# Kernel tuning notes

Measured on AMD Instinct MI355X. Metric: run time of the kernel, lower is better.

Reference implementation:

```python
import jax, jax.numpy as jnp
import numpy as np

N, E, H, F, ED, IN = 50000, 800000, 4, 32, 5, 256
NEG_SLOPE = 0.2


def setup_inputs() -> dict:
    key = jax.random.key(0)
    ks = jax.random.split(key, 13)
    s = 0.05
    return {
        "feat": jax.random.normal(ks[0], (N, IN), jnp.float32),
        "edge_fea": jax.random.normal(ks[1], (E, ED), jnp.float32),
        "src": jax.random.randint(ks[2], (E,), 0, N, dtype=jnp.int32),
        "dst": jax.random.randint(ks[3], (E,), 0, N, dtype=jnp.int32),
        "W_fc": jax.random.normal(ks[4], (IN, H * F), jnp.float32) * s,
        "W_edg": jax.random.normal(ks[5], (ED, H * ED), jnp.float32) * s,
        "b_edg": jnp.zeros((H * ED,), jnp.float32),
        "attn_l": jax.random.normal(ks[6], (1, H, F), jnp.float32) * s,
        "attn_r": jax.random.normal(ks[7], (1, H, F), jnp.float32) * s,
        "attn_edg": jax.random.normal(ks[8], (1, H, ED), jnp.float32) * s,
        "W_out": jax.random.normal(ks[9], (ED + F, F), jnp.float32) * s,
        "b_out": jnp.zeros((F,), jnp.float32),
        "bias": jnp.zeros((H * F,), jnp.float32),
    }


def reference(feat, edge_fea, src, dst, W_fc, W_edg, b_edg,
              attn_l, attn_r, attn_edg, W_out, b_out, bias):
    # node projection: [N, IN] -> [N, H, F]
    feat_src = (feat @ W_fc).reshape(N, H, F)
    # edge projection: [E, ED] -> [E, H, ED]
    efe = (edge_fea @ W_edg + b_edg).reshape(E, H, ED)
    # per-head attention logits
    el = (feat_src * attn_l).sum(-1)          # [N, H]
    er = (feat_src * attn_r).sum(-1)          # [N, H]
    ee = (efe * attn_edg).sum(-1)             # [E, H]
    e = jax.nn.leaky_relu(el[src] + er[dst] + ee, NEG_SLOPE)  # [E, H]
    # edge softmax over incoming edges of each dst node (numerically stable)
    m = jax.ops.segment_max(e, dst, num_segments=N)            # [N, H]
    ex = jnp.exp(e - m[dst])
    den = jax.ops.segment_sum(ex, dst, num_segments=N)         # [N, H]
    a = (ex / den[dst])[:, :, None]                            # [E, H, 1]
    # two weighted scatter-aggregations
    ft_f = jax.ops.segment_sum(a * efe, dst, num_segments=N)             # [N, H, ED]
    ft = jax.ops.segment_sum(a * feat_src[src], dst, num_segments=N)     # [N, H, F]
    rst = jnp.concatenate([ft_f, ft], axis=-1) @ W_out + b_out           # [N, H, F]
    rst = rst + bias.reshape(1, H, F)
    return rst
```

## Files before the change

kernel.cpp:

```cpp
#include <hip/hip_runtime.h>
#include <hip/hip_fp16.h>

#define N_NODES 50000
#define E_EDGES 800000
#define H_HEADS 4
#define F_FEAT 32
#define ED_DIM 5
#define IN_DIM 256
#define HF 128
#define NEG_SLOPE 0.2f
#define MAXD 64
#define PAYD 48
#define NPB 16
#define PROJ_BLOCKS 782
#define SCAT_BLOCKS 3125

typedef _Float16 half8 __attribute__((ext_vector_type(8)));
typedef float floatx4 __attribute__((ext_vector_type(4)));

__global__ __launch_bounds__(64) void k_wconv(
    const float* __restrict__ W_fc,
    _Float16* __restrict__ Whi, _Float16* __restrict__ Wlo,
    int* __restrict__ cnt)
{
    int b = blockIdx.x;
    int l = threadIdx.x;
    for (int i = b * 64 + l; i < N_NODES; i += 64 * 64) cnt[i] = 0;
    int kt = b >> 3, nt = b & 7;
    int kbase = kt * 32 + (l >> 4) * 8;
    int n = nt * 16 + (l & 15);
    half8 hi, lo;
#pragma unroll
    for (int j = 0; j < 8; ++j) {
        float w = W_fc[(kbase + j) * HF + n];
        _Float16 h = (_Float16)w;
        hi[j] = h;
        lo[j] = (_Float16)(w - (float)h);
    }
    size_t off = ((size_t)b * 64 + l) * 8;
    *(half8*)(Whi + off) = hi;
    *(half8*)(Wlo + off) = lo;
}

template <bool PAY>
__global__ __launch_bounds__(256) void k_scat(
    const int* __restrict__ dst,
    const int* __restrict__ src,
    const float* __restrict__ edge_fea,
    int* __restrict__ cnt,
    int* __restrict__ slots,
    char* __restrict__ pay)
{
    int e = blockIdx.x * 256 + threadIdx.x;
    if (e >= E_EDGES) return;
    int d = dst[e];
    if constexpr (PAY) {
        int s = src[e];
        const float* ep = edge_fea + (size_t)e * 5;
        float ef0 = ep[0], ef1 = ep[1], ef2 = ep[2], ef3 = ep[3], ef4 = ep[4];
        __half2 q01 = __floats2half2_rn(ef0, ef1);
        __half2 q23 = __floats2half2_rn(ef2, ef3);
        __half2 q4  = __floats2half2_rn(ef4, 0.f);
        int pos = atomicAdd(&cnt[d], 1);
        if (pos < PAYD) {
            uint4 v;
            v.x = *(unsigned*)&q01;
            v.y = *(unsigned*)&q23;
            v.z = *(unsigned*)&q4;
            v.w = (unsigned)s;
            *(uint4*)(pay + ((size_t)d * PAYD + pos) * 16) = v;
        }
    } else {
        int pos = atomicAdd(&cnt[d], 1);
        if (pos < MAXD) slots[(size_t)d * MAXD + pos] = e;
    }
}

__global__ __launch_bounds__(256) void k_proj(
    const float* __restrict__ feat,
    const _Float16* __restrict__ Whi,
    const _Float16* __restrict__ Wlo,
    const float* __restrict__ attn_l,
    const float* __restrict__ attn_r,
    __half2* __restrict__ feat_src,
    float* __restrict__ el,
    float* __restrict__ er)
{
    __shared__ _Float16 sC[4][16][136];

    int t = threadIdx.x;
    int lane = t & 63, wv = t >> 6;
    int l15 = lane & 15, lq = lane >> 4;
    int n0 = blockIdx.x * 64 + wv * 16;
    int arow = n0 + l15;
    int ar = arow < N_NODES ? arow : 0;

    floatx4 acc[8];
#pragma unroll
    for (int i = 0; i < 8; ++i) acc[i] = (floatx4){0.f, 0.f, 0.f, 0.f};

    const float4* Arow = (const float4*)(feat + (size_t)ar * IN_DIM);
    const half8* BH = (const half8*)Whi;
    const half8* BL = (const half8*)Wlo;
    int abase = lq * 2;

    for (int ks = 0; ks < 8; ++ks) {
        float4 a0 = Arow[ks * 8 + abase];
        float4 a1 = Arow[ks * 8 + abase + 1];
        float av[8] = {a0.x, a0.y, a0.z, a0.w, a1.x, a1.y, a1.z, a1.w};
        half8 ahi, alo;
#pragma unroll
        for (int j = 0; j < 8; ++j) {
            _Float16 h = (_Float16)av[j];
            ahi[j] = h;
            alo[j] = (_Float16)(av[j] - (float)h);
        }
#pragma unroll
        for (int tt = 0; tt < 8; ++tt) {
            half8 bh = BH[(ks * 8 + tt) * 64 + lane];
            half8 bl = BL[(ks * 8 + tt) * 64 + lane];
            acc[tt] = __builtin_amdgcn_mfma_f32_16x16x32_f16(ahi, bh, acc[tt], 0, 0, 0);
            acc[tt] = __builtin_amdgcn_mfma_f32_16x16x32_f16(alo, bh, acc[tt], 0, 0, 0);
            acc[tt] = __builtin_amdgcn_mfma_f32_16x16x32_f16(ahi, bl, acc[tt], 0, 0, 0);
        }
    }

#pragma unroll
    for (int tt = 0; tt < 8; ++tt) {
        int c = tt * 16 + l15;
#pragma unroll
        for (int r = 0; r < 4; ++r)
            sC[wv][lq * 4 + r][c] = (_Float16)acc[tt][r];
    }
    __syncthreads();

    int lr = lane >> 2;
    int hh = lane & 3;
    int n = n0 + lr;
    const _Float16* crow = &sC[wv][lr][hh * 32];
    const float* alp = attn_l + hh * 32;
    const float* arp = attn_r + hh * 32;
    float pl = 0.f, pr = 0.f;
#pragma unroll
    for (int i = 0; i < 32; ++i) {
        float v = (float)crow[i];
        pl += v * alp[i];
        pr += v * arp[i];
    }
    if (n < N_NODES) {
        el[n * H_HEADS + hh] = pl;
        er[n * H_HEADS + hh] = pr;
        uint4* po = (uint4*)(feat_src + (size_t)n * 64 + hh * 16);
        const uint4* ps = (const uint4*)crow;
        po[0] = ps[0]; po[1] = ps[1]; po[2] = ps[2]; po[3] = ps[3];
    }
}

__device__ __forceinline__ void acc8f(float* acc, uint4 v, float a) {
    float2 f;
    f = __half22float2(*(__half2*)&v.x); acc[0] += a * f.x; acc[1] += a * f.y;
    f = __half22float2(*(__half2*)&v.y); acc[2] += a * f.x; acc[3] += a * f.y;
    f = __half22float2(*(__half2*)&v.z); acc[4] += a * f.x; acc[5] += a * f.y;
    f = __half22float2(*(__half2*)&v.w); acc[6] += a * f.x; acc[7] += a * f.y;
}

template <bool PAY>
__global__ __launch_bounds__(256) void k_gather_out(
    const int* __restrict__ cnt, const int* __restrict__ slots,
    const char* __restrict__ pay,
    const int* __restrict__ src,
    const float* __restrict__ edge_fea,
    const float* __restrict__ el, const float* __restrict__ er,
    const __half2* __restrict__ feat_src,
    const float* __restrict__ W_edg, const float* __restrict__ b_edg,
    const float* __restrict__ attn_edg,
    const float* __restrict__ W_out, const float* __restrict__ b_out,
    const float* __restrict__ bias,
    float* __restrict__ out)
{
    constexpr int PD   = PAY ? PAYD : MAXD;
    constexpr int SAVR = PAY ? 200  : 264;
    constexpr int SSR  = PAY ? 50   : 66;

    __shared__ float sWe[100], sBe[20], sA[20], sWo[37 * 32], sBo[32], sBi[128];
    __shared__ __align__(16) __half          sav[NPB * SAVR];
    __shared__ __align__(16) unsigned short ssrc[NPB * SSR];
    __shared__ __align__(16) __half          sft[NPB * 136];
    int t = threadIdx.x;
    if (t < 100) sWe[t] = W_edg[t];
    if (t < 20) { sBe[t] = b_edg[t]; sA[t] = attn_edg[t]; }
    for (int i = t; i < 37 * 32; i += 256) sWo[i] = W_out[i];
    if (t < 32)  sBo[t] = b_out[t];
    if (t < 128) sBi[t] = bias[t];
    __syncthreads();

    int lane = t & 63;
    int wv   = t >> 6;
    int q    = lane >> 4;
    int ql   = lane & 15;
    int nb   = wv * 4 + q;
    int n    = blockIdx.x * NPB + nb;
    int h    = ql >> 2;

    int dq = cnt[n]; if (dq > PD) dq = PD;

    if (ql == 0) ssrc[nb * SSR] = 0;
    if (ql < 4)  sav[nb * SAVR + ql] = __float2half(0.f);

    float4 ern = ((const float4*)er)[n];

    float WA[5][4], cst[4];
#pragma unroll
    for (int hh = 0; hh < 4; hh++) {
        float c0 = 0.f;
#pragma unroll
        for (int dd = 0; dd < 5; dd++) c0 += sBe[hh * 5 + dd] * sA[hh * 5 + dd];
        cst[hh] = c0;
#pragma unroll
        for (int i = 0; i < 5; i++) {
            float w = 0.f;
#pragma unroll
            for (int dd = 0; dd < 5; dd++) w += sWe[i * 20 + hh * 5 + dd] * sA[hh * 5 + dd];
            WA[i][hh] = w;
        }
    }

    int dmax = dq;
    { int o = __shfl_xor(dmax, 16); dmax = dmax > o ? dmax : o;
      o = __shfl_xor(dmax, 32);     dmax = dmax > o ? dmax : o; }

    float sa4[4] = {0.f, 0.f, 0.f, 0.f};
    float m[20];
#pragma unroll
    for (int i = 0; i < 20; i++) m[i] = 0.f;

    for (int r = 0; r < dmax; r += 16) {
        int idx = r + ql;
        if (idx < dq) {
            float ef0, ef1, ef2, ef3, ef4;
            int s;
            if constexpr (PAY) {
                uint4 p = ((const uint4*)pay)[(size_t)n * PAYD + idx];
                float2 f01 = __half22float2(*(__half2*)&p.x);
                float2 f23 = __half22float2(*(__half2*)&p.y);
                float2 f4x = __half22float2(*(__half2*)&p.z);
                ef0 = f01.x; ef1 = f01.y; ef2 = f23.x; ef3 = f23.y; ef4 = f4x.x;
                s = (int)p.w;
            } else {
                int e = slots[(size_t)n * MAXD + idx];
                s = src[e];
                const float* ep = edge_fea + (size_t)e * 5;
                ef0 = ep[0]; ef1 = ep[1]; ef2 = ep[2]; ef3 = ep[3]; ef4 = ep[4];
            }
            float b0 = cst[0] + ef0*WA[0][0] + ef1*WA[1][0] + ef2*WA[2][0] + ef3*WA[3][0] + ef4*WA[4][0];
            float b1 = cst[1] + ef0*WA[0][1] + ef1*WA[1][1] + ef2*WA[2][1] + ef3*WA[3][1] + ef4*WA[4][1];
            float b2 = cst[2] + ef0*WA[0][2] + ef1*WA[1][2] + ef2*WA[2][2] + ef3*WA[3][2] + ef4*WA[4][2];
            float b3 = cst[3] + ef0*WA[0][3] + ef1*WA[1][3] + ef2*WA[2][3] + ef3*WA[3][3] + ef4*WA[4][3];
            float4 els = ((const float4*)el)[s];
            float lv0 = els.x + ern.x + b0;
            float lv1 = els.y + ern.y + b1;
            float lv2 = els.z + ern.z + b2;
            float lv3 = els.w + ern.w + b3;
            lv0 = lv0 >= 0.f ? lv0 : NEG_SLOPE * lv0;
            lv1 = lv1 >= 0.f ? lv1 : NEG_SLOPE * lv1;
            lv2 = lv2 >= 0.f ? lv2 : NEG_SLOPE * lv2;
            lv3 = lv3 >= 0.f ? lv3 : NEG_SLOPE * lv3;
            float a0 = __expf(lv0), a1 = __expf(lv1), a2 = __expf(lv2), a3 = __expf(lv3);
            sa4[0] += a0; sa4[1] += a1; sa4[2] += a2; sa4[3] += a3;
            m[0]  += a0 * ef0; m[1]  += a0 * ef1; m[2]  += a0 * ef2; m[3]  += a0 * ef3; m[4]  += a0 * ef4;
            m[5]  += a1 * ef0; m[6]  += a1 * ef1; m[7]  += a1 * ef2; m[8]  += a1 * ef3; m[9]  += a1 * ef4;
            m[10] += a2 * ef0; m[11] += a2 * ef1; m[12] += a2 * ef2; m[13] += a2 * ef3; m[14] += a2 * ef4;
            m[15] += a3 * ef0; m[16] += a3 * ef1; m[17] += a3 * ef2; m[18] += a3 * ef3; m[19] += a3 * ef4;
            ssrc[nb * SSR + idx] = (unsigned short)s;
            __half2 p01 = __floats2half2_rn(a0, a1);
            __half2 p23 = __floats2half2_rn(a2, a3);
            uint2 pk = make_uint2(*(unsigned*)&p01, *(unsigned*)&p23);
            *(uint2*)&sav[nb * SAVR + idx * 4] = pk;
        }
    }

    float acc[8];
#pragma unroll
    for (int k = 0; k < 8; k++) acc[k] = 0.f;
    const uint4* fs4 = (const uint4*)feat_src;
    int savb = nb * SAVR + h;
    int sib  = nb * SSR;

    for (int j = 0; j < dmax; j += 8) {
        int cc[8]; float aa[8]; int ss[8]; uint4 vv[8];
#pragma unroll
        for (int u = 0; u < 8; ++u) {
            int jj = j + u;
            cc[u] = (jj < dq) ? jj : 0;
            aa[u] = (jj < dq) ? __half2float(sav[savb + cc[u] * 4]) : 0.f;
        }
#pragma unroll
        for (int u = 0; u < 8; ++u) ss[u] = ssrc[sib + cc[u]];
#pragma unroll
        for (int u = 0; u < 8; ++u) vv[u] = fs4[(size_t)ss[u] * 16 + ql];
#pragma unroll
        for (int u = 0; u < 8; ++u) acc8f(acc, vv[u], aa[u]);
    }

#pragma unroll
    for (int off = 1; off < 16; off <<= 1) {
#pragma unroll
        for (int hh = 0; hh < 4; hh++) sa4[hh] += __shfl_xor(sa4[hh], off);
#pragma unroll
        for (int qq = 0; qq < 20; qq++) m[qq] += __shfl_xor(m[qq], off);
    }
    float rh = sa4[h] > 0.f ? 1.f / sa4[h] : 0.f;
#pragma unroll
    for (int k = 0; k < 8; k++) acc[k] *= rh;

    {
        __half2 h01 = __floats2half2_rn(acc[0], acc[1]);
        __half2 h23 = __floats2half2_rn(acc[2], acc[3]);
        __half2 h45 = __floats2half2_rn(acc[4], acc[5]);
        __half2 h67 = __floats2half2_rn(acc[6], acc[7]);
        uint4 pk = make_uint4(*(unsigned*)&h01, *(unsigned*)&h23,
                              *(unsigned*)&h45, *(unsigned*)&h67);
        *(uint4*)&sft[nb * 136 + 8 * ql] = pk;
    }

    float ftf[5];
#pragma unroll
    for (int d = 0; d < 5; d++) {
        float s = 0.f;
#pragma unroll
        for (int i = 0; i < 5; i++) s += m[h * 5 + i] * sWe[i * 20 + h * 5 + d];
        ftf[d] = (dq > 0) ? (sBe[h * 5 + d] + s * rh) : 0.f;
    }

    int f0 = 8 * (ql & 3);
    float o[8];
#pragma unroll
    for (int k = 0; k < 8; k++) {
        int f = f0 + k, cc = h * 32 + f;
        o[k] = sBo[f] + sBi[cc];
#pragma unroll
        for (int d = 0; d < 5; d++) o[k] += ftf[d] * sWo[d * 32 + f];
    }
    for (int g = 0; g < 32; g++) {
        float ftg = __half2float(sft[nb * 136 + h * 32 + g]);
#pragma unroll
        for (int k = 0; k < 8; k++) o[k] += ftg * sWo[(5 + g) * 32 + f0 + k];
    }
    float4* po = (float4*)(out + (size_t)n * HF + 8 * ql);
    po[0] = make_float4(o[0], o[1], o[2], o[3]);
    po[1] = make_float4(o[4], o[5], o[6], o[7]);
}

extern "C" void kernel_launch(void* const* d_in, const int* in_sizes, int n_in,
                              void* d_out, int out_size, void* d_ws, size_t ws_size,
                              hipStream_t stream) {
    const float* feat     = (const float*)d_in[0];
    const float* edge_fea = (const float*)d_in[1];
    const int*   src      = (const int*)d_in[2];
    const int*   dst      = (const int*)d_in[3];
    const float* W_fc     = (const float*)d_in[4];
    const float* W_edg    = (const float*)d_in[5];
    const float* b_edg    = (const float*)d_in[6];
    const float* attn_l   = (const float*)d_in[7];
    const float* attn_r   = (const float*)d_in[8];
    const float* attn_edg = (const float*)d_in[9];
    const float* W_out    = (const float*)d_in[10];
    const float* b_out    = (const float*)d_in[11];
    const float* bias     = (const float*)d_in[12];

    char* ws = (char*)d_ws;
    size_t off = 0;
    __half2* feat_src = (__half2*)(ws + off); off += (size_t)N_NODES * 128 * 2;
    float*   el       = (float*)(ws + off);   off += (size_t)N_NODES * 4 * 4;
    float*   er       = (float*)(ws + off);   off += (size_t)N_NODES * 4 * 4;
    int*     cnt      = (int*)(ws + off);     off += (size_t)N_NODES * 4;
    _Float16* Whi     = (_Float16*)(ws + off); off += 8 * 8 * 64 * 8 * 2;
    _Float16* Wlo     = (_Float16*)(ws + off); off += 8 * 8 * 64 * 8 * 2;
    size_t off_common = off;
    char* pay = ws + off_common;
    size_t need_pay = off_common + (size_t)N_NODES * PAYD * 16;
    int* slots = (int*)(ws + off_common);

    bool use_pay = ws_size >= need_pay;

    k_wconv<<<64, 64, 0, stream>>>(W_fc, Whi, Wlo, cnt);
    if (use_pay) {
        k_scat<true><<<SCAT_BLOCKS, 256, 0, stream>>>(dst, src, edge_fea, cnt, slots, pay);
        k_proj<<<PROJ_BLOCKS, 256, 0, stream>>>(feat, Whi, Wlo, attn_l, attn_r,
                                                feat_src, el, er);
        k_gather_out<true><<<N_NODES / NPB, 256, 0, stream>>>(
            cnt, slots, pay, src, edge_fea, el, er, feat_src,
            W_edg, b_edg, attn_edg, W_out, b_out, bias, (float*)d_out);
    } else {
        k_scat<false><<<SCAT_BLOCKS, 256, 0, stream>>>(dst, src, edge_fea, cnt, slots, pay);
        k_proj<<<PROJ_BLOCKS, 256, 0, stream>>>(feat, Whi, Wlo, attn_l, attn_r,
                                                feat_src, el, er);
        k_gather_out<false><<<N_NODES / NPB, 256, 0, stream>>>(
            cnt, slots, pay, src, edge_fea, el, er, feat_src,
            W_edg, b_edg, attn_edg, W_out, b_out, bias, (float*)d_out);
    }
}
```

Measured before the change: 283.3 us.

## Merge edge scatter and node projection into one launch with disjoint block ranges

The edge-bucketing scatter kernel and the node projection GEMM kernel become one kernel: the first block range does the scatter and the rest run the projection. The two independent stages can now overlap on the GPU and one launch gap goes away. Each scatter thread now handles four edges instead of one, with all loads issued before the atomics for more memory-level parallelism. The fused kernel carries the projection's shared-memory allocation for every block, which may lower occupancy for the scatter blocks.

```diff
diff --git a/kernel.cpp b/kernel.cpp
--- a/kernel.cpp
+++ b/kernel.cpp
@@ -13,7 +13,8 @@
 #define PAYD 48
 #define NPB 16
 #define PROJ_BLOCKS 782
-#define SCAT_BLOCKS 3125
+#define SCATB 782
+#define FUSED_BLOCKS (SCATB + PROJ_BLOCKS)
 
 typedef _Float16 half8 __attribute__((ext_vector_type(8)));
 typedef float floatx4 __attribute__((ext_vector_type(4)));
@@ -43,55 +44,75 @@
 }
 
 template <bool PAY>
-__global__ __launch_bounds__(256) void k_scat(
-    const int* __restrict__ dst,
-    const int* __restrict__ src,
-    const float* __restrict__ edge_fea,
-    int* __restrict__ cnt,
-    int* __restrict__ slots,
-    char* __restrict__ pay)
-{
-    int e = blockIdx.x * 256 + threadIdx.x;
-    if (e >= E_EDGES) return;
-    int d = dst[e];
-    if constexpr (PAY) {
-        int s = src[e];
-        const float* ep = edge_fea + (size_t)e * 5;
-        float ef0 = ep[0], ef1 = ep[1], ef2 = ep[2], ef3 = ep[3], ef4 = ep[4];
-        __half2 q01 = __floats2half2_rn(ef0, ef1);
-        __half2 q23 = __floats2half2_rn(ef2, ef3);
-        __half2 q4  = __floats2half2_rn(ef4, 0.f);
-        int pos = atomicAdd(&cnt[d], 1);
-        if (pos < PAYD) {
-            uint4 v;
-            v.x = *(unsigned*)&q01;
-            v.y = *(unsigned*)&q23;
-            v.z = *(unsigned*)&q4;
-            v.w = (unsigned)s;
-            *(uint4*)(pay + ((size_t)d * PAYD + pos) * 16) = v;
-        }
-    } else {
-        int pos = atomicAdd(&cnt[d], 1);
-        if (pos < MAXD) slots[(size_t)d * MAXD + pos] = e;
-    }
-}
-
-__global__ __launch_bounds__(256) void k_proj(
+__global__ __launch_bounds__(256) void k_fused(
     const float* __restrict__ feat,
     const _Float16* __restrict__ Whi,
     const _Float16* __restrict__ Wlo,
     const float* __restrict__ attn_l,
     const float* __restrict__ attn_r,
+    const int* __restrict__ dst,
+    const int* __restrict__ src,
+    const float* __restrict__ edge_fea,
     __half2* __restrict__ feat_src,
     float* __restrict__ el,
-    float* __restrict__ er)
+    float* __restrict__ er,
+    int* __restrict__ cnt,
+    int* __restrict__ slots,
+    char* __restrict__ pay)
 {
     __shared__ _Float16 sC[4][16][136];
+
+    int bid = blockIdx.x;
+    if (bid < SCATB) {
+        int tid = threadIdx.x;
+        int base = bid * 1024 + tid;
+        int e[4], d[4], pos[4];
+        bool val[4];
+        uint4 pv[4];
+#pragma unroll
+        for (int u = 0; u < 4; ++u) {
+            e[u] = base + u * 256;
+            val[u] = e[u] < E_EDGES;
+            int ec = val[u] ? e[u] : 0;
+            d[u] = dst[ec];
+        }
+        if constexpr (PAY) {
+#pragma unroll
+            for (int u = 0; u < 4; ++u) {
+                int ec = val[u] ? e[u] : 0;
+                int s = src[ec];
+                const float* ep = edge_fea + (size_t)ec * 5;
+                __half2 q01 = __floats2half2_rn(ep[0], ep[1]);
+                __half2 q23 = __floats2half2_rn(ep[2], ep[3]);
+                __half2 q4  = __floats2half2_rn(ep[4], 0.f);
+                pv[u].x = *(unsigned*)&q01;
+                pv[u].y = *(unsigned*)&q23;
+                pv[u].z = *(unsigned*)&q4;
+                pv[u].w = (unsigned)s;
+            }
+        }
+#pragma unroll
+        for (int u = 0; u < 4; ++u)
+            pos[u] = val[u] ? atomicAdd(&cnt[d[u]], 1) : 0x7fffffff;
+        if constexpr (PAY) {
+#pragma unroll
+            for (int u = 0; u < 4; ++u)
+                if (pos[u] < PAYD)
+                    *(uint4*)(pay + ((size_t)d[u] * PAYD + pos[u]) * 16) = pv[u];
+        } else {
+#pragma unroll
+            for (int u = 0; u < 4; ++u)
+                if (pos[u] < MAXD) slots[(size_t)d[u] * MAXD + pos[u]] = e[u];
+        }
+        return;
+    }
+
+    int pid = bid - SCATB;
 
     int t = threadIdx.x;
     int lane = t & 63, wv = t >> 6;
     int l15 = lane & 15, lq = lane >> 4;
-    int n0 = blockIdx.x * 64 + wv * 16;
+    int n0 = pid * 64 + wv * 16;
     int arow = n0 + l15;
     int ar = arow < N_NODES ? arow : 0;
 
@@ -385,16 +406,16 @@
 
     k_wconv<<<64, 64, 0, stream>>>(W_fc, Whi, Wlo, cnt);
     if (use_pay) {
-        k_scat<true><<<SCAT_BLOCKS, 256, 0, stream>>>(dst, src, edge_fea, cnt, slots, pay);
-        k_proj<<<PROJ_BLOCKS, 256, 0, stream>>>(feat, Whi, Wlo, attn_l, attn_r,
-                                                feat_src, el, er);
+        k_fused<true><<<FUSED_BLOCKS, 256, 0, stream>>>(
+            feat, Whi, Wlo, attn_l, attn_r, dst, src, edge_fea,
+            feat_src, el, er, cnt, slots, pay);
         k_gather_out<true><<<N_NODES / NPB, 256, 0, stream>>>(
             cnt, slots, pay, src, edge_fea, el, er, feat_src,
             W_edg, b_edg, attn_edg, W_out, b_out, bias, (float*)d_out);
     } else {
-        k_scat<false><<<SCAT_BLOCKS, 256, 0, stream>>>(dst, src, edge_fea, cnt, slots, pay);
-        k_proj<<<PROJ_BLOCKS, 256, 0, stream>>>(feat, Whi, Wlo, attn_l, attn_r,
-                                                feat_src, el, er);
+        k_fused<false><<<FUSED_BLOCKS, 256, 0, stream>>>(
+            feat, Whi, Wlo, attn_l, attn_r, dst, src, edge_fea,
+            feat_src, el, er, cnt, slots, pay);
         k_gather_out<false><<<N_NODES / NPB, 256, 0, stream>>>(
             cnt, slots, pay, src, edge_fea, el, er, feat_src,
             W_edg, b_edg, attn_edg, W_out, b_out, bias, (float*)d_out);
```

Result: faster. 273.8 us (-3.4%).

## Merge edge scatter and node projection into one heterogeneous kernel launch

Applied to the files above, without the earlier changes.

The edge bucketing scatter and the MFMA node projection used to be two separate launches. They are now one grid: the first PROJ_BLOCKS blocks run the projection and the remaining blocks run the scatter. This removes a launch and its serialization gap, and lets the atomic-heavy scatter overlap with the compute-bound projection. Scatter blocks still declare the projection's shared-memory tile, which may reduce their occupancy.

```diff
diff --git a/kernel.cpp b/kernel.cpp
--- a/kernel.cpp
+++ b/kernel.cpp
@@ -43,49 +43,49 @@
 }
 
 template <bool PAY>
-__global__ __launch_bounds__(256) void k_scat(
-    const int* __restrict__ dst,
-    const int* __restrict__ src,
-    const float* __restrict__ edge_fea,
-    int* __restrict__ cnt,
-    int* __restrict__ slots,
-    char* __restrict__ pay)
-{
-    int e = blockIdx.x * 256 + threadIdx.x;
-    if (e >= E_EDGES) return;
-    int d = dst[e];
-    if constexpr (PAY) {
-        int s = src[e];
-        const float* ep = edge_fea + (size_t)e * 5;
-        float ef0 = ep[0], ef1 = ep[1], ef2 = ep[2], ef3 = ep[3], ef4 = ep[4];
-        __half2 q01 = __floats2half2_rn(ef0, ef1);
-        __half2 q23 = __floats2half2_rn(ef2, ef3);
-        __half2 q4  = __floats2half2_rn(ef4, 0.f);
-        int pos = atomicAdd(&cnt[d], 1);
-        if (pos < PAYD) {
-            uint4 v;
-            v.x = *(unsigned*)&q01;
-            v.y = *(unsigned*)&q23;
-            v.z = *(unsigned*)&q4;
-            v.w = (unsigned)s;
-            *(uint4*)(pay + ((size_t)d * PAYD + pos) * 16) = v;
-        }
-    } else {
-        int pos = atomicAdd(&cnt[d], 1);
-        if (pos < MAXD) slots[(size_t)d * MAXD + pos] = e;
-    }
-}
-
-__global__ __launch_bounds__(256) void k_proj(
+__global__ __launch_bounds__(256) void k_proj_scatter(
     const float* __restrict__ feat,
     const _Float16* __restrict__ Whi,
     const _Float16* __restrict__ Wlo,
     const float* __restrict__ attn_l,
     const float* __restrict__ attn_r,
+    const int* __restrict__ dst,
+    const int* __restrict__ src,
+    const float* __restrict__ edge_fea,
     __half2* __restrict__ feat_src,
     float* __restrict__ el,
-    float* __restrict__ er)
+    float* __restrict__ er,
+    int* __restrict__ cnt,
+    int* __restrict__ slots,
+    char* __restrict__ pay)
 {
+    if (blockIdx.x >= PROJ_BLOCKS) {
+        int e = (blockIdx.x - PROJ_BLOCKS) * 256 + threadIdx.x;
+        if (e < E_EDGES) {
+            int d = dst[e];
+            if constexpr (PAY) {
+                int s = src[e];
+                const float* ep = edge_fea + (size_t)e * 5;
+                __half2 q01 = __floats2half2_rn(ep[0], ep[1]);
+                __half2 q23 = __floats2half2_rn(ep[2], ep[3]);
+                __half2 q4  = __floats2half2_rn(ep[4], 0.f);
+                int pos = atomicAdd(&cnt[d], 1);
+                if (pos < PAYD) {
+                    uint4 v;
+                    v.x = *(unsigned*)&q01;
+                    v.y = *(unsigned*)&q23;
+                    v.z = *(unsigned*)&q4;
+                    v.w = (unsigned)s;
+                    *(uint4*)(pay + ((size_t)d * PAYD + pos) * 16) = v;
+                }
+            } else {
+                int pos = atomicAdd(&cnt[d], 1);
+                if (pos < MAXD) slots[(size_t)d * MAXD + pos] = e;
+            }
+        }
+        return;
+    }
+
     __shared__ _Float16 sC[4][16][136];
 
     int t = threadIdx.x;
@@ -385,16 +385,16 @@
 
     k_wconv<<<64, 64, 0, stream>>>(W_fc, Whi, Wlo, cnt);
     if (use_pay) {
-        k_scat<true><<<SCAT_BLOCKS, 256, 0, stream>>>(dst, src, edge_fea, cnt, slots, pay);
-        k_proj<<<PROJ_BLOCKS, 256, 0, stream>>>(feat, Whi, Wlo, attn_l, attn_r,
-                                                feat_src, el, er);
+        k_proj_scatter<true><<<PROJ_BLOCKS + SCAT_BLOCKS, 256, 0, stream>>>(
+            feat, Whi, Wlo, attn_l, attn_r, dst, src, edge_fea,
+            feat_src, el, er, cnt, slots, pay);
         k_gather_out<true><<<N_NODES / NPB, 256, 0, stream>>>(
             cnt, slots, pay, src, edge_fea, el, er, feat_src,
             W_edg, b_edg, attn_edg, W_out, b_out, bias, (float*)d_out);
     } else {
-        k_scat<false><<<SCAT_BLOCKS, 256, 0, stream>>>(dst, src, edge_fea, cnt, slots, pay);
-        k_proj<<<PROJ_BLOCKS, 256, 0, stream>>>(feat, Whi, Wlo, attn_l, attn_r,
-                                                feat_src, el, er);
+        k_proj_scatter<false><<<PROJ_BLOCKS + SCAT_BLOCKS, 256, 0, stream>>>(
+            feat, Whi, Wlo, attn_l, attn_r, dst, src, edge_fea,
+            feat_src, el, er, cnt, slots, pay);
         k_gather_out<false><<<N_NODES / NPB, 256, 0, stream>>>(
             cnt, slots, pay, src, edge_fea, el, er, feat_src,
             W_edg, b_edg, attn_edg, W_out, b_out, bias, (float*)d_out);
```

Measured after the change: 253.6 us. 10.5% less time.
